# Performance work log

Measured on AMD Instinct MI355X. Metric: run time of the kernel, lower is better.

The kernel has to match this reference:

```python
import jax, jax.numpy as jnp
import numpy as np

B, D, NN = 16, 2, 100        # batch, num_depots, num_nodes (pickups+deliveries)
N2 = NN // 2                 # pickups (= deliveries)
NA = D + NN                  # total nodes per batch graph
H, HE, L = 128, 64, 3        # hidden_node_dim, hidden_edge_dim, conv_layers
SLOPE, EPS = 0.2, 1e-5


def _bn(x, g, b):
    # BatchNorm1d in training mode: per-feature batch stats (biased var)
    m = jnp.mean(x, axis=0)
    v = jnp.var(x, axis=0)
    return (x - m) * jax.lax.rsqrt(v + EPS) * g + b


def _leaky(x):
    return jnp.where(x >= 0, x, SLOPE * x)


def _prop(xk, e, m, Wg):
    # Dense-equivalent of GatConv.propagate over a fully-connected per-batch grid.
    # Edge (i, j): x_i = x[target j], x_j = x[source i] (matches edge_index layout:
    # row0 = i repeated, row1 = j blockwise; PyG target = edge_index[1]).
    # xk: [B, N, H] transformed node feats; e: [B, N, N, HE]; m: [B, N, N] 0/1.
    h = xk.shape[-1]
    wi, wj, we = Wg[:h], Wg[h:2 * h], Wg[2 * h:]  # split cat([x_i, x_j, e]) @ Wg
    alpha = _leaky((xk @ wi)[:, None, :, :]        # x_i contribution (target j)
                   + (xk @ wj)[:, :, None, :]      # x_j contribution (source i)
                   + jnp.einsum('bijc,ch->bijh', e, we))
    alpha = jnp.where(m[..., None] != 0, alpha, -jnp.inf)
    alpha = jax.nn.softmax(alpha, axis=1)          # segment softmax keyed by target j
    return jnp.einsum('bijh,bih->bjh', alpha, xk)  # scatter-add x_j * alpha to targets


def _forward(x, demand, time_window, edge_attr_d, edge_attr_r,
             W0, W1, W2, W3, W4,
             b0_g, b0_b, b1_g, b1_b, b2_g, b2_b, b3_g, b3_b, b4_g, b4_b,
             ff_w1, ff_b1, ff_w2, ff_b2, bn_g, bn_b,
             Wvla, Wvlp, Wvld, Wga, Wgp, Wgd,
             edge_index, mask_adjacency_d, mask_adjacency_r):
    ds = jnp.concatenate([x, demand, time_window], axis=-1)  # [B, NA, 5]
    dep = _bn(ds[:, :D].reshape(B * D, -1) @ W0, b0_g, b0_b).reshape(B, D, H)
    pk_in = jnp.concatenate([ds[:, D:D + N2], ds[:, D + N2:D + NN]], axis=-1).reshape(B * N2, -1)
    pk = _bn(pk_in @ W1, b1_g, b1_b).reshape(B, N2, H)
    dl = _bn(ds[:, D + N2:D + NN].reshape(B * N2, -1) @ W2, b2_g, b2_b).reshape(B, N2, H)
    e_d = _bn(edge_attr_d.reshape(-1, edge_attr_d.shape[-1]) @ W3, b3_g, b3_b).reshape(B, NA, NA, HE)
    e_r = _bn(edge_attr_r.reshape(-1, edge_attr_r.shape[-1]) @ W4, b4_g, b4_b).reshape(B, NA, NA, HE)
    m_d = mask_adjacency_d.reshape(B, NA, NA)
    m_r = mask_adjacency_r.reshape(B, NA, NA)

    def conv(xc, e, m, l):
        xall = xc @ Wvla[l]
        pick = xc[:, D:D + N2] @ Wvlp[l]
        deli = xc[:, D + N2:D + NN] @ Wvld[l]
        X1 = _prop(xall, e, m, Wga[l])
        X2 = _prop(pick, e[:, D:D + N2, D:D + N2], m[:, D:D + N2, D:D + N2], Wgp[l])
        X3 = _prop(deli, e[:, D + N2:D + NN, D + N2:D + NN], m[:, D + N2:D + NN, D + N2:D + NN], Wgd[l])
        # faithful to torch.cat(dim=0) followed by view(B, -1, H)
        Xc = jnp.concatenate([X1.reshape(-1, H), X2.reshape(-1, H), X3.reshape(-1, H)], axis=0).reshape(B, -1, H)
        xa, xp, xdd = Xc[:, :NA], Xc[:, NA:NA + N2], Xc[:, NA + N2:NA + NN]
        return jnp.concatenate([xa[:, :D], xa[:, D:D + N2] + xp, xa[:, D + N2:] + xdd], axis=1)

    xd = jnp.concatenate([dep, pk, dl], axis=1)  # [B, NA, H]
    xr = xd
    for l in range(L):
        xd, xr = conv(xd, e_d, m_d, l), conv(xr, e_r, m_r, l)

    def ff_bn(xc):
        xf = xc.reshape(-1, H)
        f = jax.nn.relu(xf @ ff_w1 + ff_b1) @ ff_w2 + ff_b2
        return _bn(xf + f, bn_g, bn_b).reshape(B, NA, H)

    return ff_bn(xd), ff_bn(xr)


def setup_inputs() -> dict:
    key = jax.random.key(0)
    it = iter(jax.random.split(key, 40))

    def nrm(shape, s=0.05):
        return (s * jax.random.normal(next(it), shape)).astype(jnp.float32)

    def uni(shape):
        return jax.random.uniform(next(it), shape, dtype=jnp.float32)

    x = nrm((B, NA, 2), 1.0)
    # first D entries per batch are depots (demand == 0), rest are nonzero
    demand = jnp.concatenate([jnp.zeros((B, D, 1), jnp.float32), uni((B, NN, 1)) + 0.5], axis=1)
    time_window = uni((B, NA, 2))
    edge_attr_d = uni((B, NA * NA, 2))
    edge_attr_r = uni((B, NA * NA, 2))
    eye = jnp.eye(NA, dtype=jnp.int32)[None]
    mask_d = jnp.maximum(jax.random.randint(next(it), (B, NA, NA), 0, 2, dtype=jnp.int32), eye).reshape(B, NA * NA)
    mask_r = jnp.maximum(jax.random.randint(next(it), (B, NA, NA), 0, 2, dtype=jnp.int32), eye).reshape(B, NA * NA)
    ii = jnp.arange(B * NA, dtype=jnp.int32)
    edge_index = jnp.stack([jnp.repeat(ii, NA), jnp.repeat(ii.reshape(B, NA), NA, axis=0).reshape(-1)])

    inp = dict(
        x=x, demand=demand, time_window=time_window,
        edge_attr_d=edge_attr_d, edge_attr_r=edge_attr_r,
        W0=nrm((5, H)), W1=nrm((10, H)), W2=nrm((5, H)), W3=nrm((2, HE)), W4=nrm((2, HE)),
        b0_g=jnp.ones(H, jnp.float32), b0_b=jnp.zeros(H, jnp.float32),
        b1_g=jnp.ones(H, jnp.float32), b1_b=jnp.zeros(H, jnp.float32),
        b2_g=jnp.ones(H, jnp.float32), b2_b=jnp.zeros(H, jnp.float32),
        b3_g=jnp.ones(HE, jnp.float32), b3_b=jnp.zeros(HE, jnp.float32),
        b4_g=jnp.ones(HE, jnp.float32), b4_b=jnp.zeros(HE, jnp.float32),
        ff_w1=nrm((H, H)), ff_b1=jnp.zeros(H, jnp.float32),
        ff_w2=nrm((H, H)), ff_b2=jnp.zeros(H, jnp.float32),
        bn_g=jnp.ones(H, jnp.float32), bn_b=jnp.zeros(H, jnp.float32),
        Wvla=nrm((L, H, H)), Wvlp=nrm((L, H, H)), Wvld=nrm((L, H, H)),
        Wga=nrm((L, 2 * H + HE, H)), Wgp=nrm((L, 2 * H + HE, H)), Wgd=nrm((L, 2 * H + HE, H)),
        edge_index=edge_index, mask_adjacency_d=mask_d, mask_adjacency_r=mask_r,
    )
    return inp


def reference(x, demand, time_window, edge_attr_d, edge_attr_r,
              W0, W1, W2, W3, W4,
              b0_g, b0_b, b1_g, b1_b, b2_g, b2_b, b3_g, b3_b, b4_g, b4_b,
              ff_w1, ff_b1, ff_w2, ff_b2, bn_g, bn_b,
              Wvla, Wvlp, Wvld, Wga, Wgp, Wgd,
              edge_index, mask_adjacency_d, mask_adjacency_r):
    return _forward(x, demand, time_window, edge_attr_d, edge_attr_r,
                    W0, W1, W2, W3, W4,
                    b0_g, b0_b, b1_g, b1_b, b2_g, b2_b, b3_g, b3_b, b4_g, b4_b,
                    ff_w1, ff_b1, ff_w2, ff_b2, bn_g, bn_b,
                    Wvla, Wvlp, Wvld, Wga, Wgp, Wgd,
                    edge_index, mask_adjacency_d, mask_adjacency_r)
```

## Files before the change

kernel.cpp:

```cpp
#include <hip/hip_runtime.h>
#include <stdint.h>

#define B 16
#define D 2
#define NN 100
#define N2 50
#define NA 102
#define H 128
#define HE 64
#define L 3
#define SLOPE 0.2f
#define EPS 1e-5f

#define NAE (NA*NA)
#define EN (B*NAE)
#define R1 (B*NA)
#define R2 (B*N2)
#define RV (R1 + 2*R2)
#define NC 202
#define TI 18

#define MOM_PART  0
#define NODE_PART 1280
#define ACC_FF    27392
#define OFF_PQR   27904
#define OFF_X0    34816
#define OFF_V     (OFF_X0 + R1*H)
#define OFF_AB    (OFF_V + 2*RV*H)
#define OFF_XA    (OFF_AB + 2*RV*2*H)
#define OFF_XL    (OFF_XA + 4*RV*H)
#define OFF_Z     (OFF_XL + 4*RV*H)

struct KParams {
    const float *x, *dm, *tw, *ead, *ear;
    const float *W0, *W1, *W2, *W3, *W4;
    const float *b0g, *b0b, *b1g, *b1b, *b2g, *b2b, *b3g, *b3b, *b4g, *b4b;
    const float *ffw1, *ffb1, *ffw2, *ffb2, *bng, *bnb;
    const float *Wvla, *Wvlp, *Wvld, *Wga, *Wgp, *Wgd;
    const int *mask_d, *mask_r;
    float *ws, *out;
};

__device__ __forceinline__ void decode_vrow(int ridx, int& b, int& node) {
    if (ridx < R1) { b = ridx / NA; node = ridx % NA; }
    else if (ridx < R1 + R2) { int p = ridx - R1; b = p / N2; node = D + p % N2; }
    else { int p = ridx - R1 - R2; b = p / N2; node = D + N2 + p % N2; }
}
__device__ __forceinline__ void decode_nrow(int vr, int& b, int& node) {
    if (vr < 32) { b = vr >> 1; node = vr & 1; }
    else if (vr < 832) { int p = vr - 32; b = p / N2; node = D + p % N2; }
    else { int p = vr - 832; b = p / N2; node = D + N2 + p % N2; }
}
__device__ __forceinline__ float combined_parts(const float* __restrict__ ws, int g, int b, int node, int k) {
    const float* XA = ws + OFF_XA;
    const float* XL = ws + OFF_XL;
    int r = g*RV + b*NC + node;
    int s = 2*RV;
    float a = XA[r*H + k] + XA[(r + s)*H + k];
    float l = XL[r*H + k] + XL[(r + s)*H + k];
    float v = a / l;
    if (node >= D) {
        int r2 = r + 100;
        float a2 = XA[r2*H + k] + XA[(r2 + s)*H + k];
        float l2 = XL[r2*H + k] + XL[(r2 + s)*H + k];
        v += a2 / l2;
    }
    return v;
}

__global__ __launch_bounds__(256) void kf_A(KParams p) {
    __shared__ float sd[256];
    int u = blockIdx.x, tid = threadIdx.x;
    if (u < 256) {
        int g = u >> 7, bb = u & 127;
        const float2* ea = (const float2*)(g ? p.ear : p.ead);
        float s0 = 0, s1 = 0, s00 = 0, s11 = 0, s01 = 0;
        for (int idx = bb*256 + tid; idx < EN; idx += 128*256) {
            float2 v = ea[idx];
            s0 += v.x; s1 += v.y; s00 += v.x*v.x; s11 += v.y*v.y; s01 += v.x*v.y;
        }
        float vals[5] = {s0, s1, s00, s11, s01};
        for (int q = 0; q < 5; q++) {
            sd[tid] = vals[q];
            __syncthreads();
            for (int off = 128; off > 0; off >>= 1) {
                if (tid < off) sd[tid] += sd[tid + off];
                __syncthreads();
            }
            if (tid == 0) p.ws[MOM_PART + (g*128 + bb)*5 + q] = sd[0];
            __syncthreads();
        }
    } else if (u < 307) {
        int half = tid >> 7, c = tid & 127;
        int vb = (u - 256)*2 + half;
        int seg = (vb < 2) ? 0 : (vb < 52 ? 1 : 2);
        const float* W = seg == 0 ? p.W0 : (seg == 1 ? p.W1 : p.W2);
        int nf = seg == 1 ? 10 : 5;
        float w[10];
        for (int f = 0; f < nf; f++) w[f] = W[f*H + c];
        float* x0 = p.ws + OFF_X0;
        float ls = 0, lss = 0;
        for (int r = 0; r < 16; r++) {
            int vr = vb*16 + r;
            int b, node; decode_nrow(vr, b, node);
            int row = b*NA + node;
            float y = p.x[row*2]*w[0] + p.x[row*2+1]*w[1] + p.dm[row]*w[2]
                    + p.tw[row*2]*w[3] + p.tw[row*2+1]*w[4];
            if (seg == 1) {
                int r2 = row + N2;
                y += p.x[r2*2]*w[5] + p.x[r2*2+1]*w[6] + p.dm[r2]*w[7]
                   + p.tw[r2*2]*w[8] + p.tw[r2*2+1]*w[9];
            }
            x0[row*H + c] = y;
            ls += y; lss += y*y;
        }
        p.ws[NODE_PART + vb*256 + c] = ls;
        p.ws[NODE_PART + vb*256 + 128 + c] = lss;
    } else {
        for (int i = tid; i < 512; i += 256) p.ws[ACC_FF + i] = 0.0f;
    }
}

__global__ __launch_bounds__(128) void kf_pqr(KParams p) {
    int u = blockIdx.x;
    int g = u / 9, rem = u % 9, seg = rem / 3, lay = rem % 3;
    __shared__ float st[192];
    __shared__ float momsh[5];
    int t = threadIdx.x;
    if (t < 5) {
        float s = 0;
        for (int q = 0; q < 128; q++) s += p.ws[MOM_PART + (g*128 + q)*5 + t];
        momsh[t] = s;
    }
    __syncthreads();
    if (t < 64) {
        const float* W  = g ? p.W4 : p.W3;
        const float* gv = g ? p.b4g : p.b3g;
        const float* bv = g ? p.b4b : p.b3b;
        float Nr = (float)EN;
        float S0 = momsh[0], S1 = momsh[1], S00 = momsh[2], S11 = momsh[3], S01 = momsh[4];
        float w0 = W[t], w1 = W[64 + t];
        float m = (S0*w0 + S1*w1) / Nr;
        float E2 = (S00*w0*w0 + 2.0f*S01*w0*w1 + S11*w1*w1) / Nr;
        float var = E2 - m*m;
        float s = gv[t] * rsqrtf(var + EPS);
        st[t] = w0 * s; st[64 + t] = w1 * s; st[128 + t] = bv[t] - m*s;
    }
    __syncthreads();
    int h = t;
    const float* Wg = (seg == 0 ? p.Wga : (seg == 1 ? p.Wgp : p.Wgd)) + lay*320*H;
    float P = 0, Q = 0, Rr = 0;
    for (int cc = 0; cc < HE; cc++) {
        float w = Wg[(2*H + cc)*H + h];
        P += st[cc]*w; Q += st[64 + cc]*w; Rr += st[128 + cc]*w;
    }
    float* o = p.ws + OFF_PQR + ((g*3 + seg)*3 + lay)*384;
    o[h] = P; o[128 + h] = Q; o[256 + h] = Rr;
}

__global__ __launch_bounds__(256) void kf_gemm(KParams p, int lay) {
    __shared__ float xs[8*H];
    __shared__ float vs[8*H];
    __shared__ float scs[3*128], shs[3*128];
    int g = blockIdx.x / 404, tb = blockIdx.x % 404;
    int rowbase = tb * 8;
    int tid = threadIdx.x;
    float* ws = p.ws;
    if (lay == 0 && tid < 128) {
        int c = tid;
        #pragma unroll
        for (int seg = 0; seg < 3; seg++) {
            int lo = seg == 0 ? 0 : (seg == 1 ? 2 : 52);
            int hi = seg == 0 ? 2 : (seg == 1 ? 52 : 102);
            float s = 0, ss = 0;
            for (int q = lo; q < hi; q++) {
                s  += ws[NODE_PART + q*256 + c];
                ss += ws[NODE_PART + q*256 + 128 + c];
            }
            float cnt = seg == 0 ? 32.0f : 800.0f;
            float m = s / cnt, v = ss / cnt - m*m;
            const float* gp = seg == 0 ? p.b0g : (seg == 1 ? p.b1g : p.b2g);
            const float* bp = seg == 0 ? p.b0b : (seg == 1 ? p.b1b : p.b2b);
            float sc = gp[c] * rsqrtf(v + EPS);
            scs[seg*128 + c] = sc;
            shs[seg*128 + c] = bp[c] - m*sc;
        }
    }
    __syncthreads();
    const float* x0 = ws + OFF_X0;
    for (int e = 0; e < 4; e++) {
        int lin = tid + e*256;
        int r = lin >> 7, k = lin & 127;
        int b, node; decode_vrow(rowbase + r, b, node);
        float val;
        if (lay == 0) {
            int s3 = node < D ? 0 : (node < D + N2 ? 1 : 2);
            val = x0[(b*NA + node)*H + k] * scs[s3*128 + k] + shs[s3*128 + k];
        } else {
            val = combined_parts(ws, g, b, node, k);
        }
        xs[r*H + k] = val;
    }
    __syncthreads();
    int seg = tb < 204 ? 0 : (tb < 304 ? 1 : 2);
    const float* W = (seg == 0 ? p.Wvla : (seg == 1 ? p.Wvlp : p.Wvld)) + lay*H*H;
    int col = tid & 127, half = tid >> 7;
    float acc[4] = {0,0,0,0};
    const float* Wp = W + col;
    float w0 = Wp[0], w1 = Wp[H], w2 = Wp[2*H], w3 = Wp[3*H];
    for (int k4 = 0; k4 < 32; k4++) {
        int kn = ((k4 + 1) & 31) * 4;
        const float* q = Wp + kn*H;
        float n0 = q[0], n1 = q[H], n2 = q[2*H], n3 = q[3*H];
        #pragma unroll
        for (int rr = 0; rr < 4; rr++) {
            float4 x4 = *(const float4*)&xs[(half + rr*2)*H + 4*k4];
            acc[rr] = fmaf(x4.w, w3, fmaf(x4.z, w2, fmaf(x4.y, w1, fmaf(x4.x, w0, acc[rr]))));
        }
        w0 = n0; w1 = n1; w2 = n2; w3 = n3;
    }
    float* V = ws + OFF_V + g*RV*H;
    #pragma unroll
    for (int rr = 0; rr < 4; rr++) {
        vs[(half + rr*2)*H + col] = acc[rr];
        V[(rowbase + half + rr*2)*H + col] = acc[rr];
    }
    __syncthreads();
    const float* Wg = (seg == 0 ? p.Wga : (seg == 1 ? p.Wgp : p.Wgd)) + lay*320*H;
    const float* wb = Wg + ((tid >> 7) * H) * H + (tid & 127);
    float a2[8];
    #pragma unroll
    for (int rr = 0; rr < 8; rr++) a2[rr] = 0.0f;
    float v0 = wb[0], v1 = wb[H], v2 = wb[2*H], v3 = wb[3*H];
    for (int k4 = 0; k4 < 32; k4++) {
        int kn = ((k4 + 1) & 31) * 4;
        const float* q = wb + kn*H;
        float n0 = q[0], n1 = q[H], n2 = q[2*H], n3 = q[3*H];
        #pragma unroll
        for (int rr = 0; rr < 8; rr++) {
            float4 x4 = *(const float4*)&vs[rr*H + 4*k4];
            a2[rr] = fmaf(x4.w, v3, fmaf(x4.z, v2, fmaf(x4.y, v1, fmaf(x4.x, v0, a2[rr]))));
        }
        v0 = n0; v1 = n1; v2 = n2; v3 = n3;
    }
    float* AB = ws + OFF_AB + g*RV*2*H;
    #pragma unroll
    for (int rr = 0; rr < 8; rr++) AB[(rowbase + rr)*256 + tid] = a2[rr];
}

__global__ __launch_bounds__(256, 6) void kf_attn(KParams p, int lay) {
    __shared__ float2 Bs[TI*64];
    __shared__ float2 Vs[TI*64];
    __shared__ float2 se[4*52];
    __shared__ int    msk[52];
    int kx = blockIdx.x, y = blockIdx.y;
    int ih = y & 1, jq = (y >> 1) & 1, y3 = y >> 2;
    int ci = y3 / 27, r = y3 % 27;
    int combo = kx + 8*ci;
    int g = combo >> 4, b = combo & 15;
    int seg, jg, n, o, base;
    if (r < 13)      { seg = 0; jg = r;      n = NA; o = 0;      base = 0; }
    else if (r < 20) { seg = 1; jg = r - 13; n = N2; o = D;      base = R1; }
    else             { seg = 2; jg = r - 20; n = N2; o = D + N2; base = R1 + R2; }
    int j0 = jg*8 + jq*4;
    int tid = threadIdx.x;
    int c = tid & 63, wv = tid >> 6;
    int j = j0 + wv;
    bool jok = j < n;
    int nh0 = (n + 1) >> 1;
    int i0 = ih * nh0;
    int cnt = min(nh0, n - i0);

    float* ws = p.ws;
    const float* pqr = ws + OFF_PQR + ((g*3 + seg)*3 + lay)*384;
    float2 Pv = ((const float2*)pqr)[c];
    float2 Qv = ((const float2*)(pqr + 128))[c];
    float2 Rv = ((const float2*)(pqr + 256))[c];
    const float2* ea = (const float2*)(g ? p.ear : p.ead);
    const int* mask = g ? p.mask_r : p.mask_d;
    const float* V  = ws + OFF_V  + g*RV*H   + base*H;
    const float* AB = ws + OFF_AB + g*RV*2*H + base*2*H;

    if (tid < cnt) {
        int i = i0 + tid;
        int ibase = b*NAE + (o + i)*NA + o + j0;
        int bits = 0;
        #pragma unroll
        for (int jj = 0; jj < 4; jj++) {
            int valid = (j0 + jj < n) ? (mask[ibase + jj] != 0) : 0;
            bits |= valid << jj;
            se[jj*52 + tid] = valid ? ea[ibase + jj] : make_float2(0.f, 0.f);
        }
        msk[tid] = bits;
    }

    float Ax = 0.f, Ay = 0.f;
    if (jok) {
        float2 Aj = ((const float2*)&AB[(b*n + j)*256])[c];
        Ax = Aj.x + Rv.x; Ay = Aj.y + Rv.y;
    }
    float2 lsum = make_float2(0.f, 0.f), asum = make_float2(0.f, 0.f);

    for (int t0 = 0; t0 < cnt; t0 += TI) {
        int rows = min(TI, cnt - t0);
        __syncthreads();
        for (int idx = tid; idx < rows*64; idx += 256) {
            int ir = idx >> 6, cc = idx & 63;
            int gi = b*n + i0 + t0 + ir;
            Bs[ir*64 + cc] = *(const float2*)&AB[gi*256 + 128 + 2*cc];
            Vs[ir*64 + cc] = *(const float2*)&V[gi*128 + 2*cc];
        }
        __syncthreads();
        if (jok) {
            for (int ir = 0; ir < rows; ir++) {
                int ii = t0 + ir;
                if (!((msk[ii] >> wv) & 1)) continue;
                float2 Bi = Bs[ir*64 + c];
                float2 Vi = Vs[ir*64 + c];
                float2 ev = se[wv*52 + ii];
                float tx = fmaf(ev.x, Pv.x, fmaf(ev.y, Qv.x, Ax + Bi.x));
                float ty = fmaf(ev.x, Pv.y, fmaf(ev.y, Qv.y, Ay + Bi.y));
                tx = fminf(fmaxf(tx, SLOPE*tx), 80.0f);
                ty = fminf(fmaxf(ty, SLOPE*ty), 80.0f);
                float px = __expf(tx), py = __expf(ty);
                lsum.x += px; lsum.y += py;
                asum.x = fmaf(px, Vi.x, asum.x);
                asum.y = fmaf(py, Vi.y, asum.y);
            }
        }
    }
    if (jok) {
        int rowW = (ih*2 + g)*RV + base + b*n + j;
        ((float2*)&ws[OFF_XA + rowW*H])[c] = asum;
        ((float2*)&ws[OFF_XL + rowW*H])[c] = lsum;
    }
}

__global__ __launch_bounds__(256) void kf_ff(KParams p) {
    __shared__ float xs[8*H];
    __shared__ float hs[8*H];
    int g = blockIdx.x / 204, tb = blockIdx.x % 204;
    int rowbase = tb * 8;
    int tid = threadIdx.x;
    float* ws = p.ws;
    for (int e = 0; e < 4; e++) {
        int lin = tid + e*256;
        int r = lin >> 7, k = lin & 127;
        int ridx = rowbase + r;
        int b = ridx / NA, node = ridx % NA;
        xs[r*H + k] = combined_parts(ws, g, b, node, k);
    }
    __syncthreads();
    int col = tid & 127, half = tid >> 7;
    float acc[4] = {0,0,0,0};
    const float* W1p = p.ffw1 + col;
    float w0 = W1p[0], w1 = W1p[H], w2 = W1p[2*H], w3 = W1p[3*H];
    for (int k4 = 0; k4 < 32; k4++) {
        int kn = ((k4 + 1) & 31) * 4;
        const float* q = W1p + kn*H;
        float n0 = q[0], n1 = q[H], n2 = q[2*H], n3 = q[3*H];
        #pragma unroll
        for (int rr = 0; rr < 4; rr++) {
            float4 x4 = *(const float4*)&xs[(half + rr*2)*H + 4*k4];
            acc[rr] = fmaf(x4.w, w3, fmaf(x4.z, w2, fmaf(x4.y, w1, fmaf(x4.x, w0, acc[rr]))));
        }
        w0 = n0; w1 = n1; w2 = n2; w3 = n3;
    }
    float b1 = p.ffb1[col];
    #pragma unroll
    for (int rr = 0; rr < 4; rr++) {
        float hv = acc[rr] + b1;
        hs[(half + rr*2)*H + col] = hv > 0.0f ? hv : 0.0f;
    }
    __syncthreads();
    #pragma unroll
    for (int rr = 0; rr < 4; rr++) acc[rr] = 0.0f;
    const float* W2p = p.ffw2 + col;
    w0 = W2p[0]; w1 = W2p[H]; w2 = W2p[2*H]; w3 = W2p[3*H];
    for (int k4 = 0; k4 < 32; k4++) {
        int kn = ((k4 + 1) & 31) * 4;
        const float* q = W2p + kn*H;
        float n0 = q[0], n1 = q[H], n2 = q[2*H], n3 = q[3*H];
        #pragma unroll
        for (int rr = 0; rr < 4; rr++) {
            float4 x4 = *(const float4*)&hs[(half + rr*2)*H + 4*k4];
            acc[rr] = fmaf(x4.w, w3, fmaf(x4.z, w2, fmaf(x4.y, w1, fmaf(x4.x, w0, acc[rr]))));
        }
        w0 = n0; w1 = n1; w2 = n2; w3 = n3;
    }
    float b2 = p.ffb2[col];
    float* Z = ws + OFF_Z + g*R1*H;
    float ls = 0, lss = 0;
    #pragma unroll
    for (int rr = 0; rr < 4; rr++) {
        int row = rowbase + half + rr*2;
        float z = acc[rr] + b2 + xs[(half + rr*2)*H + col];
        Z[row*H + col] = z;
        ls += z; lss += z*z;
    }
    atomicAdd(&ws[ACC_FF + g*256 + col], ls);
    atomicAdd(&ws[ACC_FF + g*256 + 128 + col], lss);
}

__global__ __launch_bounds__(256) void kf_f3(KParams p) {
    int e = blockIdx.x * 256 + threadIdx.x;
    if (e >= 2*R1*H) return;
    int g = e / (R1*H);
    int c = e & 127;
    float m = p.ws[ACC_FF + g*256 + c] / 1632.0f;
    float v = p.ws[ACC_FF + g*256 + 128 + c] / 1632.0f - m*m;
    float sc = p.bng[c] * rsqrtf(v + EPS);
    float sh = p.bnb[c] - m*sc;
    p.out[e] = p.ws[OFF_Z + e] * sc + sh;
}

extern "C" void kernel_launch(void* const* d_in, const int* in_sizes, int n_in,
                              void* d_out, int out_size, void* d_ws, size_t ws_size,
                              hipStream_t stream) {
    KParams p;
    p.x    = (const float*)d_in[0];
    p.dm   = (const float*)d_in[1];
    p.tw   = (const float*)d_in[2];
    p.ead  = (const float*)d_in[3];
    p.ear  = (const float*)d_in[4];
    p.W0   = (const float*)d_in[5];
    p.W1   = (const float*)d_in[6];
    p.W2   = (const float*)d_in[7];
    p.W3   = (const float*)d_in[8];
    p.W4   = (const float*)d_in[9];
    p.b0g  = (const float*)d_in[10];
    p.b0b  = (const float*)d_in[11];
    p.b1g  = (const float*)d_in[12];
    p.b1b  = (const float*)d_in[13];
    p.b2g  = (const float*)d_in[14];
    p.b2b  = (const float*)d_in[15];
    p.b3g  = (const float*)d_in[16];
    p.b3b  = (const float*)d_in[17];
    p.b4g  = (const float*)d_in[18];
    p.b4b  = (const float*)d_in[19];
    p.ffw1 = (const float*)d_in[20];
    p.ffb1 = (const float*)d_in[21];
    p.ffw2 = (const float*)d_in[22];
    p.ffb2 = (const float*)d_in[23];
    p.bng  = (const float*)d_in[24];
    p.bnb  = (const float*)d_in[25];
    p.Wvla = (const float*)d_in[26];
    p.Wvlp = (const float*)d_in[27];
    p.Wvld = (const float*)d_in[28];
    p.Wga  = (const float*)d_in[29];
    p.Wgp  = (const float*)d_in[30];
    p.Wgd  = (const float*)d_in[31];
    p.mask_d = (const int*)d_in[33];
    p.mask_r = (const int*)d_in[34];
    p.ws  = (float*)d_ws;
    p.out = (float*)d_out;

    kf_A  <<<308, 256, 0, stream>>>(p);
    kf_pqr<<<18, 128, 0, stream>>>(p);
    for (int lay = 0; lay < L; lay++) {
        kf_gemm<<<808, 256, 0, stream>>>(p, lay);
        kf_attn<<<dim3(8, 432), 256, 0, stream>>>(p, lay);
    }
    kf_ff<<<408, 256, 0, stream>>>(p);
    kf_f3<<<1632, 256, 0, stream>>>(p);
}
```

Baseline: 316.6 us.

## Fuse init kernels, give each attention thread two targets, simplify GEMM weight loads

The edge-moment reduction and the PQR projection are merged into one init kernel. Each of its 18 blocks now reduces the full edge tensor alone instead of using 128 partial blocks, which removes a launch but cuts parallelism for that reduction and repeats the read across blocks. The attention kernel now assigns two target columns per wave, which halves its grid and reuses the B and V tiles loaded into shared memory, and it drops the occupancy hint from its launch bounds. The GEMM loops replace manual software prefetch with plain loads and unroll 4, and the final BN kernel uses a grid-stride loop with fewer blocks.

```diff
diff --git a/kernel.cpp b/kernel.cpp
--- a/kernel.cpp
+++ b/kernel.cpp
@@ -20,7 +20,6 @@
 #define NC 202
 #define TI 18
 
-#define MOM_PART  0
 #define NODE_PART 1280
 #define ACC_FF    27392
 #define OFF_PQR   27904
@@ -68,14 +67,16 @@
     return v;
 }
 
-__global__ __launch_bounds__(256) void kf_A(KParams p) {
-    __shared__ float sd[256];
+__global__ __launch_bounds__(256) void kf_init(KParams p) {
     int u = blockIdx.x, tid = threadIdx.x;
-    if (u < 256) {
-        int g = u >> 7, bb = u & 127;
+    if (u < 18) {
+        int g = u / 9, rem = u % 9, seg = rem / 3, lay = rem % 3;
+        __shared__ float sd[256];
+        __shared__ float st[192];
+        __shared__ float mom[5];
         const float2* ea = (const float2*)(g ? p.ear : p.ead);
         float s0 = 0, s1 = 0, s00 = 0, s11 = 0, s01 = 0;
-        for (int idx = bb*256 + tid; idx < EN; idx += 128*256) {
+        for (int idx = tid; idx < EN; idx += 256) {
             float2 v = ea[idx];
             s0 += v.x; s1 += v.y; s00 += v.x*v.x; s11 += v.y*v.y; s01 += v.x*v.y;
         }
@@ -87,12 +88,36 @@
                 if (tid < off) sd[tid] += sd[tid + off];
                 __syncthreads();
             }
-            if (tid == 0) p.ws[MOM_PART + (g*128 + bb)*5 + q] = sd[0];
+            if (tid == 0) mom[q] = sd[0];
             __syncthreads();
         }
-    } else if (u < 307) {
+        if (tid < 64) {
+            const float* W  = g ? p.W4 : p.W3;
+            const float* gv = g ? p.b4g : p.b3g;
+            const float* bv = g ? p.b4b : p.b3b;
+            float Nr = (float)EN;
+            float w0 = W[tid], w1 = W[64 + tid];
+            float m = (mom[0]*w0 + mom[1]*w1) / Nr;
+            float E2 = (mom[2]*w0*w0 + 2.0f*mom[4]*w0*w1 + mom[3]*w1*w1) / Nr;
+            float var = E2 - m*m;
+            float s = gv[tid] * rsqrtf(var + EPS);
+            st[tid] = w0 * s; st[64 + tid] = w1 * s; st[128 + tid] = bv[tid] - m*s;
+        }
+        __syncthreads();
+        if (tid < 128) {
+            int h = tid;
+            const float* Wg = (seg == 0 ? p.Wga : (seg == 1 ? p.Wgp : p.Wgd)) + lay*320*H;
+            float P = 0, Q = 0, Rr = 0;
+            for (int cc = 0; cc < HE; cc++) {
+                float w = Wg[(2*H + cc)*H + h];
+                P += st[cc]*w; Q += st[64 + cc]*w; Rr += st[128 + cc]*w;
+            }
+            float* o = p.ws + OFF_PQR + ((g*3 + seg)*3 + lay)*384;
+            o[h] = P; o[128 + h] = Q; o[256 + h] = Rr;
+        }
+    } else if (u < 69) {
         int half = tid >> 7, c = tid & 127;
-        int vb = (u - 256)*2 + half;
+        int vb = (u - 18)*2 + half;
         int seg = (vb < 2) ? 0 : (vb < 52 ? 1 : 2);
         const float* W = seg == 0 ? p.W0 : (seg == 1 ? p.W1 : p.W2);
         int nf = seg == 1 ? 10 : 5;
@@ -121,43 +146,6 @@
     }
 }
 
-__global__ __launch_bounds__(128) void kf_pqr(KParams p) {
-    int u = blockIdx.x;
-    int g = u / 9, rem = u % 9, seg = rem / 3, lay = rem % 3;
-    __shared__ float st[192];
-    __shared__ float momsh[5];
-    int t = threadIdx.x;
-    if (t < 5) {
-        float s = 0;
-        for (int q = 0; q < 128; q++) s += p.ws[MOM_PART + (g*128 + q)*5 + t];
-        momsh[t] = s;
-    }
-    __syncthreads();
-    if (t < 64) {
-        const float* W  = g ? p.W4 : p.W3;
-        const float* gv = g ? p.b4g : p.b3g;
-        const float* bv = g ? p.b4b : p.b3b;
-        float Nr = (float)EN;
-        float S0 = momsh[0], S1 = momsh[1], S00 = momsh[2], S11 = momsh[3], S01 = momsh[4];
-        float w0 = W[t], w1 = W[64 + t];
-        float m = (S0*w0 + S1*w1) / Nr;
-        float E2 = (S00*w0*w0 + 2.0f*S01*w0*w1 + S11*w1*w1) / Nr;
-        float var = E2 - m*m;
-        float s = gv[t] * rsqrtf(var + EPS);
-        st[t] = w0 * s; st[64 + t] = w1 * s; st[128 + t] = bv[t] - m*s;
-    }
-    __syncthreads();
-    int h = t;
-    const float* Wg = (seg == 0 ? p.Wga : (seg == 1 ? p.Wgp : p.Wgd)) + lay*320*H;
-    float P = 0, Q = 0, Rr = 0;
-    for (int cc = 0; cc < HE; cc++) {
-        float w = Wg[(2*H + cc)*H + h];
-        P += st[cc]*w; Q += st[64 + cc]*w; Rr += st[128 + cc]*w;
-    }
-    float* o = p.ws + OFF_PQR + ((g*3 + seg)*3 + lay)*384;
-    o[h] = P; o[128 + h] = Q; o[256 + h] = Rr;
-}
-
 __global__ __launch_bounds__(256) void kf_gemm(KParams p, int lay) {
     __shared__ float xs[8*H];
     __shared__ float vs[8*H];
@@ -207,17 +195,14 @@
     int col = tid & 127, half = tid >> 7;
     float acc[4] = {0,0,0,0};
     const float* Wp = W + col;
-    float w0 = Wp[0], w1 = Wp[H], w2 = Wp[2*H], w3 = Wp[3*H];
+    #pragma unroll 4
     for (int k4 = 0; k4 < 32; k4++) {
-        int kn = ((k4 + 1) & 31) * 4;
-        const float* q = Wp + kn*H;
-        float n0 = q[0], n1 = q[H], n2 = q[2*H], n3 = q[3*H];
+        float w0 = Wp[(4*k4+0)*H], w1 = Wp[(4*k4+1)*H], w2 = Wp[(4*k4+2)*H], w3 = Wp[(4*k4+3)*H];
         #pragma unroll
         for (int rr = 0; rr < 4; rr++) {
             float4 x4 = *(const float4*)&xs[(half + rr*2)*H + 4*k4];
             acc[rr] = fmaf(x4.w, w3, fmaf(x4.z, w2, fmaf(x4.y, w1, fmaf(x4.x, w0, acc[rr]))));
         }
-        w0 = n0; w1 = n1; w2 = n2; w3 = n3;
     }
     float* V = ws + OFF_V + g*RV*H;
     #pragma unroll
@@ -231,42 +216,40 @@
     float a2[8];
     #pragma unroll
     for (int rr = 0; rr < 8; rr++) a2[rr] = 0.0f;
-    float v0 = wb[0], v1 = wb[H], v2 = wb[2*H], v3 = wb[3*H];
+    #pragma unroll 4
     for (int k4 = 0; k4 < 32; k4++) {
-        int kn = ((k4 + 1) & 31) * 4;
-        const float* q = wb + kn*H;
-        float n0 = q[0], n1 = q[H], n2 = q[2*H], n3 = q[3*H];
+        float v0 = wb[(4*k4+0)*H], v1 = wb[(4*k4+1)*H], v2 = wb[(4*k4+2)*H], v3 = wb[(4*k4+3)*H];
         #pragma unroll
         for (int rr = 0; rr < 8; rr++) {
             float4 x4 = *(const float4*)&vs[rr*H + 4*k4];
             a2[rr] = fmaf(x4.w, v3, fmaf(x4.z, v2, fmaf(x4.y, v1, fmaf(x4.x, v0, a2[rr]))));
         }
-        v0 = n0; v1 = n1; v2 = n2; v3 = n3;
     }
     float* AB = ws + OFF_AB + g*RV*2*H;
     #pragma unroll
     for (int rr = 0; rr < 8; rr++) AB[(rowbase + rr)*256 + tid] = a2[rr];
 }
 
-__global__ __launch_bounds__(256, 6) void kf_attn(KParams p, int lay) {
+__global__ __launch_bounds__(256) void kf_attn(KParams p, int lay) {
     __shared__ float2 Bs[TI*64];
     __shared__ float2 Vs[TI*64];
-    __shared__ float2 se[4*52];
+    __shared__ float2 se[8*52];
     __shared__ int    msk[52];
     int kx = blockIdx.x, y = blockIdx.y;
-    int ih = y & 1, jq = (y >> 1) & 1, y3 = y >> 2;
-    int ci = y3 / 27, r = y3 % 27;
+    int ih = y & 1, y2 = y >> 1;
+    int ci = y2 / 27, r = y2 % 27;
     int combo = kx + 8*ci;
     int g = combo >> 4, b = combo & 15;
     int seg, jg, n, o, base;
     if (r < 13)      { seg = 0; jg = r;      n = NA; o = 0;      base = 0; }
     else if (r < 20) { seg = 1; jg = r - 13; n = N2; o = D;      base = R1; }
     else             { seg = 2; jg = r - 20; n = N2; o = D + N2; base = R1 + R2; }
-    int j0 = jg*8 + jq*4;
+    int j0 = jg * 8;
     int tid = threadIdx.x;
     int c = tid & 63, wv = tid >> 6;
-    int j = j0 + wv;
-    bool jok = j < n;
+    int jj0 = 2*wv, jj1 = jj0 + 1;
+    int ja = j0 + jj0, jb = j0 + jj1;
+    bool oka = ja < n, okb = jb < n;
     int nh0 = (n + 1) >> 1;
     int i0 = ih * nh0;
     int cnt = min(nh0, n - i0);
@@ -286,7 +269,7 @@
         int ibase = b*NAE + (o + i)*NA + o + j0;
         int bits = 0;
         #pragma unroll
-        for (int jj = 0; jj < 4; jj++) {
+        for (int jj = 0; jj < 8; jj++) {
             int valid = (j0 + jj < n) ? (mask[ibase + jj] != 0) : 0;
             bits |= valid << jj;
             se[jj*52 + tid] = valid ? ea[ibase + jj] : make_float2(0.f, 0.f);
@@ -294,12 +277,17 @@
         msk[tid] = bits;
     }
 
-    float Ax = 0.f, Ay = 0.f;
-    if (jok) {
-        float2 Aj = ((const float2*)&AB[(b*n + j)*256])[c];
-        Ax = Aj.x + Rv.x; Ay = Aj.y + Rv.y;
-    }
-    float2 lsum = make_float2(0.f, 0.f), asum = make_float2(0.f, 0.f);
+    float A0x = 0.f, A0y = 0.f, A1x = 0.f, A1y = 0.f;
+    if (oka) {
+        float2 Aj = ((const float2*)&AB[(b*n + ja)*256])[c];
+        A0x = Aj.x + Rv.x; A0y = Aj.y + Rv.y;
+    }
+    if (okb) {
+        float2 Aj = ((const float2*)&AB[(b*n + jb)*256])[c];
+        A1x = Aj.x + Rv.x; A1y = Aj.y + Rv.y;
+    }
+    float2 l0 = make_float2(0.f, 0.f), a0 = make_float2(0.f, 0.f);
+    float2 l1 = make_float2(0.f, 0.f), a1 = make_float2(0.f, 0.f);
 
     for (int t0 = 0; t0 < cnt; t0 += TI) {
         int rows = min(TI, cnt - t0);
@@ -311,28 +299,42 @@
             Vs[ir*64 + cc] = *(const float2*)&V[gi*128 + 2*cc];
         }
         __syncthreads();
-        if (jok) {
-            for (int ir = 0; ir < rows; ir++) {
-                int ii = t0 + ir;
-                if (!((msk[ii] >> wv) & 1)) continue;
-                float2 Bi = Bs[ir*64 + c];
-                float2 Vi = Vs[ir*64 + c];
-                float2 ev = se[wv*52 + ii];
-                float tx = fmaf(ev.x, Pv.x, fmaf(ev.y, Qv.x, Ax + Bi.x));
-                float ty = fmaf(ev.x, Pv.y, fmaf(ev.y, Qv.y, Ay + Bi.y));
+        for (int ir = 0; ir < rows; ir++) {
+            int ii = t0 + ir;
+            int bits = (msk[ii] >> jj0) & 3;
+            if (!bits) continue;
+            float2 Bi = Bs[ir*64 + c];
+            float2 Vi = Vs[ir*64 + c];
+            if (bits & 1) {
+                float2 ev = se[jj0*52 + ii];
+                float tx = fmaf(ev.x, Pv.x, fmaf(ev.y, Qv.x, A0x + Bi.x));
+                float ty = fmaf(ev.x, Pv.y, fmaf(ev.y, Qv.y, A0y + Bi.y));
                 tx = fminf(fmaxf(tx, SLOPE*tx), 80.0f);
                 ty = fminf(fmaxf(ty, SLOPE*ty), 80.0f);
                 float px = __expf(tx), py = __expf(ty);
-                lsum.x += px; lsum.y += py;
-                asum.x = fmaf(px, Vi.x, asum.x);
-                asum.y = fmaf(py, Vi.y, asum.y);
-            }
-        }
-    }
-    if (jok) {
-        int rowW = (ih*2 + g)*RV + base + b*n + j;
-        ((float2*)&ws[OFF_XA + rowW*H])[c] = asum;
-        ((float2*)&ws[OFF_XL + rowW*H])[c] = lsum;
+                l0.x += px; l0.y += py;
+                a0.x = fmaf(px, Vi.x, a0.x); a0.y = fmaf(py, Vi.y, a0.y);
+            }
+            if (bits & 2) {
+                float2 ev = se[jj1*52 + ii];
+                float tx = fmaf(ev.x, Pv.x, fmaf(ev.y, Qv.x, A1x + Bi.x));
+                float ty = fmaf(ev.x, Pv.y, fmaf(ev.y, Qv.y, A1y + Bi.y));
+                tx = fminf(fmaxf(tx, SLOPE*tx), 80.0f);
+                ty = fminf(fmaxf(ty, SLOPE*ty), 80.0f);
+                float px = __expf(tx), py = __expf(ty);
+                l1.x += px; l1.y += py;
+                a1.x = fmaf(px, Vi.x, a1.x); a1.y = fmaf(py, Vi.y, a1.y);
+            }
+        }
+    }
+    int rowbaseW = (ih*2 + g)*RV + base + b*n;
+    if (oka) {
+        ((float2*)&ws[OFF_XA + (rowbaseW + ja)*H])[c] = a0;
+        ((float2*)&ws[OFF_XL + (rowbaseW + ja)*H])[c] = l0;
+    }
+    if (okb) {
+        ((float2*)&ws[OFF_XA + (rowbaseW + jb)*H])[c] = a1;
+        ((float2*)&ws[OFF_XL + (rowbaseW + jb)*H])[c] = l1;
     }
 }
 
@@ -354,17 +356,14 @@
     int col = tid & 127, half = tid >> 7;
     float acc[4] = {0,0,0,0};
     const float* W1p = p.ffw1 + col;
-    float w0 = W1p[0], w1 = W1p[H], w2 = W1p[2*H], w3 = W1p[3*H];
+    #pragma unroll 4
     for (int k4 = 0; k4 < 32; k4++) {
-        int kn = ((k4 + 1) & 31) * 4;
-        const float* q = W1p + kn*H;
-        float n0 = q[0], n1 = q[H], n2 = q[2*H], n3 = q[3*H];
+        float w0 = W1p[(4*k4+0)*H], w1 = W1p[(4*k4+1)*H], w2 = W1p[(4*k4+2)*H], w3 = W1p[(4*k4+3)*H];
         #pragma unroll
         for (int rr = 0; rr < 4; rr++) {
             float4 x4 = *(const float4*)&xs[(half + rr*2)*H + 4*k4];
             acc[rr] = fmaf(x4.w, w3, fmaf(x4.z, w2, fmaf(x4.y, w1, fmaf(x4.x, w0, acc[rr]))));
         }
-        w0 = n0; w1 = n1; w2 = n2; w3 = n3;
     }
     float b1 = p.ffb1[col];
     #pragma unroll
@@ -376,17 +375,14 @@
     #pragma unroll
     for (int rr = 0; rr < 4; rr++) acc[rr] = 0.0f;
     const float* W2p = p.ffw2 + col;
-    w0 = W2p[0]; w1 = W2p[H]; w2 = W2p[2*H]; w3 = W2p[3*H];
+    #pragma unroll 4
     for (int k4 = 0; k4 < 32; k4++) {
-        int kn = ((k4 + 1) & 31) * 4;
-        const float* q = W2p + kn*H;
-        float n0 = q[0], n1 = q[H], n2 = q[2*H], n3 = q[3*H];
+        float w0 = W2p[(4*k4+0)*H], w1 = W2p[(4*k4+1)*H], w2 = W2p[(4*k4+2)*H], w3 = W2p[(4*k4+3)*H];
         #pragma unroll
         for (int rr = 0; rr < 4; rr++) {
             float4 x4 = *(const float4*)&hs[(half + rr*2)*H + 4*k4];
             acc[rr] = fmaf(x4.w, w3, fmaf(x4.z, w2, fmaf(x4.y, w1, fmaf(x4.x, w0, acc[rr]))));
         }
-        w0 = n0; w1 = n1; w2 = n2; w3 = n3;
     }
     float b2 = p.ffb2[col];
     float* Z = ws + OFF_Z + g*R1*H;
@@ -403,15 +399,15 @@
 }
 
 __global__ __launch_bounds__(256) void kf_f3(KParams p) {
-    int e = blockIdx.x * 256 + threadIdx.x;
-    if (e >= 2*R1*H) return;
-    int g = e / (R1*H);
-    int c = e & 127;
-    float m = p.ws[ACC_FF + g*256 + c] / 1632.0f;
-    float v = p.ws[ACC_FF + g*256 + 128 + c] / 1632.0f - m*m;
-    float sc = p.bng[c] * rsqrtf(v + EPS);
-    float sh = p.bnb[c] - m*sc;
-    p.out[e] = p.ws[OFF_Z + e] * sc + sh;
+    for (int e = blockIdx.x*256 + threadIdx.x; e < 2*R1*H; e += 408*256) {
+        int g = e / (R1*H);
+        int c = e & 127;
+        float m = p.ws[ACC_FF + g*256 + c] / 1632.0f;
+        float v = p.ws[ACC_FF + g*256 + 128 + c] / 1632.0f - m*m;
+        float sc = p.bng[c] * rsqrtf(v + EPS);
+        float sh = p.bnb[c] - m*sc;
+        p.out[e] = p.ws[OFF_Z + e] * sc + sh;
+    }
 }
 
 extern "C" void kernel_launch(void* const* d_in, const int* in_sizes, int n_in,
@@ -455,12 +451,11 @@
     p.ws  = (float*)d_ws;
     p.out = (float*)d_out;
 
-    kf_A  <<<308, 256, 0, stream>>>(p);
-    kf_pqr<<<18, 128, 0, stream>>>(p);
+    kf_init<<<70, 256, 0, stream>>>(p);
     for (int lay = 0; lay < L; lay++) {
         kf_gemm<<<808, 256, 0, stream>>>(p, lay);
-        kf_attn<<<dim3(8, 432), 256, 0, stream>>>(p, lay);
+        kf_attn<<<dim3(8, 216), 256, 0, stream>>>(p, lay);
     }
     kf_ff<<<408, 256, 0, stream>>>(p);
-    kf_f3<<<1632, 256, 0, stream>>>(p);
-}
+    kf_f3<<<408, 256, 0, stream>>>(p);
+}
```

After: 491.4 us. +55.2%, slower.
